# Performance work log

Hardware: AMD Instinct MI355X
Metric: run time of the kernel (lower is better)

## Reference

```python
import jax, jax.numpy as jnp
import numpy as np

D = 256          # embedding_dim
P = 16           # padding_size (patch size, divides D)
CE = 32          # cnn_embedding_dim
HP = 4           # patch_attention_heads
HS = 4           # spatial_temporal_heads
NP = D // P      # patches per token = 16
CC = CE * HP     # conv out channels = 128


def _ln(x):
    # torch module uses mean/std (unbiased, ddof=1), no eps, no affine
    m = jnp.mean(x, axis=-1, keepdims=True)
    s = jnp.std(x, axis=-1, keepdims=True, ddof=1)
    return (x - m) / s


def setup_inputs() -> dict:
    key = jax.random.key(0)
    ks = jax.random.split(key, 20)
    def lin(k, fan_out, fan_in):
        b = 1.0 / np.sqrt(fan_in)
        kw, kb = jax.random.split(k)
        return (jax.random.uniform(kw, (fan_out, fan_in), jnp.float32, -b, b),
                jax.random.uniform(kb, (fan_out,), jnp.float32, -b, b))
    x = jax.random.normal(ks[0], (32, 512, D), jnp.float32)
    Wq, bq = lin(ks[1], D * HS, D)
    Wk, bk = lin(ks[2], D * HS, D)
    Wv, bv = lin(ks[3], D * HS, D)
    Wlin1, blin1 = lin(ks[4], D, D * HS)
    # Conv1d(1, CC, kernel=P, stride=P) weights flattened to (CC, P)
    Wqc, bqc = lin(ks[5], CC, P)
    Wkc, bkc = lin(ks[6], CC, P)
    Wvl, bvl = lin(ks[7], CC, P)
    Wlo, blo = lin(ks[8], P, CC)
    Wlout, blout = lin(ks[9], D, NP * P)
    return dict(x=x, Wq=Wq, bq=bq, Wk=Wk, bk=bk, Wv=Wv, bv=bv,
                Wlin1=Wlin1, blin1=blin1, Wqc=Wqc, bqc=bqc, Wkc=Wkc, bkc=bkc,
                Wvl=Wvl, bvl=bvl, Wlo=Wlo, blo=blo, Wlout=Wlout, blout=blout)


def reference(x, Wq, bq, Wk, bk, Wv, bv, Wlin1, blin1,
              Wqc, bqc, Wkc, bkc, Wvl, bvl, Wlo, blo, Wlout, blout):
    bs, S, _ = x.shape
    orig_x = x
    # ----- spatial-temporal multi-head attention -----
    def heads(W, b):
        y = x @ W.T + b                      # [bs,S,HS*D]
        return y.reshape(bs, S, HS, D).transpose(0, 2, 1, 3)  # [bs,HS,S,D]
    Q, K, V = heads(Wq, bq), heads(Wk, bk), heads(Wv, bv)
    att = jax.nn.softmax(jnp.einsum('bhsd,bhtd->bhst', Q, K) / D, axis=-1)
    o = jnp.einsum('bhst,bhtd->bhsd', att, V)
    o = o.transpose(0, 2, 1, 3).reshape(bs, S, HS * D)
    x1 = _ln(o @ Wlin1.T + blin1 + orig_x)
    # ----- CNN patch attention (D % P == 0, no pad branch) -----
    orig2 = x1
    xp = x1.reshape(bs * S, NP, P)           # patches per token
    # Conv1d with kernel=stride=P == per-patch linear
    Qc = (xp @ Wqc.T + bqc).reshape(-1, NP, HP, CE).transpose(0, 2, 1, 3)
    Kc = (xp @ Wkc.T + bkc).reshape(-1, NP, HP, CE).transpose(0, 2, 1, 3)
    Vc = (xp @ Wvl.T + bvl).reshape(-1, NP, HP, CE).transpose(0, 2, 1, 3)
    scale = jnp.sqrt(jnp.float32(D))
    am = jax.nn.softmax(jnp.einsum('nhpc,nhqc->nhpq', Qc, Kc) / scale, axis=-1)
    oc = jnp.einsum('nhpq,nhqc->nhpc', am, Vc)
    oc = oc.transpose(0, 2, 1, 3).reshape(-1, NP, HP * CE)
    oc = (oc @ Wlo.T + blo).reshape(-1, NP * P)
    oc = (oc @ Wlout.T + blout).reshape(bs, S, D)
    return _ln(oc + orig2)
```

## Files before the change

kernel.cpp:

```cpp
#include <hip/hip_runtime.h>
#include <hip/hip_bf16.h>
#include <math.h>


typedef __attribute__((ext_vector_type(8))) short bf16x8;
typedef __attribute__((ext_vector_type(4))) float f32x4;

__device__ __forceinline__ float bf_lo(unsigned u){ return __uint_as_float(u << 16); }
__device__ __forceinline__ float bf_hi(unsigned u){ return __uint_as_float(u & 0xFFFF0000u); }
__device__ __forceinline__ unsigned short f2bf(float f){
  unsigned u = __float_as_uint(f);
  return (unsigned short)((u + 0x7FFFu + ((u >> 16) & 1u)) >> 16);
}
__device__ __forceinline__ unsigned pack2bf(float a, float b){
  return (unsigned)f2bf(a) | ((unsigned)f2bf(b) << 16);
}
__device__ __forceinline__ bf16x8 pack8(float a0,float a1,float a2,float a3,
                                        float a4,float a5,float a6,float a7){
  union { bf16x8 v; unsigned u[4]; } t;
  t.u[0]=pack2bf(a0,a1); t.u[1]=pack2bf(a2,a3);
  t.u[2]=pack2bf(a4,a5); t.u[3]=pack2bf(a6,a7);
  return t.v;
}
__device__ __forceinline__ void gld16(const void* g, void* l){
  __builtin_amdgcn_global_load_lds((const __attribute__((address_space(1))) void*)g,
                                   (__attribute__((address_space(3))) void*)l, 16, 0, 0);
}

__global__ __launch_bounds__(256) void k_cvt(const float* __restrict__ src,
                                             unsigned short* __restrict__ dst, int n4)
{
  int i = blockIdx.x * 256 + threadIdx.x;
  if (i < n4){
    float4 v = ((const float4*)src)[i];
    ushort4 o;
    o.x = f2bf(v.x); o.y = f2bf(v.y); o.z = f2bf(v.z); o.w = f2bf(v.w);
    ((ushort4*)dst)[i] = o;
  }
}

__global__ __launch_bounds__(256) void k_packw(
    const float* __restrict__ Wqc, const float* __restrict__ Wkc,
    const float* __restrict__ Wvl, const float* __restrict__ Wlo,
    unsigned short* __restrict__ Wp)
{
  int it = blockIdx.x * 256 + threadIdx.x;
  if (it >= 1792) return;
  int ch = it >> 6, lane = it & 63;
  int g = lane >> 4, li = lane & 15;
  unsigned short o[8];
  if (ch < 24){
    int m = ch >> 3, nc = ch & 7;
    const float* W = (m == 0) ? Wqc : (m == 1 ? Wkc : Wvl);
    int c = nc * 16 + li;
    #pragma unroll
    for (int j = 0; j < 8; ++j){
      int k = g * 8 + j;
      o[j] = (k < 16) ? f2bf(W[c * 16 + k]) : (unsigned short)0;
    }
  } else {
    int kc = ch - 24;
    #pragma unroll
    for (int j = 0; j < 8; ++j){
      int k = kc * 32 + g * 8 + j;
      o[j] = f2bf(Wlo[li * 128 + k]);
    }
  }
  #pragma unroll
  for (int j = 0; j < 8; ++j) Wp[it * 8 + j] = o[j];
}

template<int EPI>
__global__ __launch_bounds__(256) void k_gemm(
    const unsigned short* __restrict__ A,
    const unsigned short* __restrict__ W,
    const float* __restrict__ b0,
    const float* __restrict__ b1,
    const float* __restrict__ b2,
    const float* __restrict__ resid,
    void* __restrict__ outp,
    unsigned short* __restrict__ Kw_,
    unsigned short* __restrict__ Vt_,
    int K)
{
  extern __shared__ char sm[];
  const int tid = threadIdx.x;
  const int wid = tid >> 6, lane = tid & 63;
  const int g = lane >> 4, li = lane & 15;
  const int wm = wid >> 1, wn = wid & 1;
  const int m0 = blockIdx.x << 7, n0 = blockIdx.y << 7;

  const unsigned short* Ab = A + (size_t)m0 * K;
  const unsigned short* Wb = W + (size_t)n0 * K;

  auto stage = [&](char* dst, const unsigned short* src, int k0){
    #pragma unroll
    for (int r = 0; r < 4; ++r){
      int row = (r << 5) + (tid >> 3);
      int cb  = (tid & 7) << 4;
      int cbs = cb ^ ((row & 7) << 4);
      gld16(src + row * K + k0 + (cbs >> 1), dst + (r << 12) + (wid << 10));
    }
  };

  f32x4 acc[4][4];
  #pragma unroll
  for (int mf = 0; mf < 4; ++mf)
    #pragma unroll
    for (int nf = 0; nf < 4; ++nf) acc[mf][nf] = (f32x4){0.f,0.f,0.f,0.f};

  const int nk = K >> 6;
  stage(sm, Ab, 0); stage(sm + 32768, Wb, 0);
  for (int kt = 0; kt < nk; ++kt){
    char* Acur = (kt & 1) ? (sm + 16384) : sm;
    char* Wcur = (kt & 1) ? (sm + 49152) : (sm + 32768);
    if (kt + 1 < nk){
      char* Anxt = (kt & 1) ? sm : (sm + 16384);
      char* Wnxt = (kt & 1) ? (sm + 32768) : (sm + 49152);
      stage(Anxt, Ab, (kt + 1) << 6);
      stage(Wnxt, Wb, (kt + 1) << 6);
    }
    __syncthreads();
    bf16x8 af[2][4], wf[2][4];
    #pragma unroll
    for (int kk = 0; kk < 2; ++kk){
      #pragma unroll
      for (int mf = 0; mf < 4; ++mf){
        int row  = (wm << 6) + (mf << 4) + li;
        int colb = ((kk << 6) + (g << 4)) ^ ((row & 7) << 4);
        af[kk][mf] = *(const bf16x8*)(Acur + (row << 7) + colb);
      }
      #pragma unroll
      for (int nf = 0; nf < 4; ++nf){
        int row  = (wn << 6) + (nf << 4) + li;
        int colb = ((kk << 6) + (g << 4)) ^ ((row & 7) << 4);
        wf[kk][nf] = *(const bf16x8*)(Wcur + (row << 7) + colb);
      }
    }
    #pragma unroll
    for (int kk = 0; kk < 2; ++kk)
      #pragma unroll
      for (int mf = 0; mf < 4; ++mf)
        #pragma unroll
        for (int nf = 0; nf < 4; ++nf)
          acc[mf][nf] = __builtin_amdgcn_mfma_f32_16x16x32_bf16(af[kk][mf], wf[kk][nf], acc[mf][nf], 0, 0, 0);
    __syncthreads();
  }

  if (EPI == 0){
    const int chunk = n0 >> 10;
    const float* bias = (chunk == 0) ? b0 : (chunk == 1 ? b1 : b2);
    const int nq0 = n0 & 1023;
    const int h = nq0 >> 8;
    if (chunk == 2){
      const int b  = m0 >> 9;
      const int bh = (b << 2) + h;
      const int d0g = (nq0 & 255) + (wn << 6);
      const int s0g = (m0 & 511) + (wm << 6);
      char* const TB = sm + (wid << 13);
      #pragma unroll
      for (int nf = 0; nf < 4; ++nf){
        const int dloc = (nf << 4) + li;
        const float bv = bias[nq0 + (wn << 6) + (nf << 4) + li];
        #pragma unroll
        for (int mf = 0; mf < 4; ++mf){
          ushort4 pk;
          pk.x = f2bf(acc[mf][nf][0] + bv); pk.y = f2bf(acc[mf][nf][1] + bv);
          pk.z = f2bf(acc[mf][nf][2] + bv); pk.w = f2bf(acc[mf][nf][3] + bv);
          const int unit = ((mf << 2) + g) ^ (dloc & 7);
          *(ushort4*)(TB + (dloc << 7) + (unit << 3)) = pk;
        }
      }
      __asm__ volatile("s_waitcnt lgkmcnt(0)" ::: "memory");
      __builtin_amdgcn_sched_barrier(0);
      #pragma unroll
      for (int p = 0; p < 8; ++p){
        const int dl = (p << 3) + (lane >> 3);
        const int u0 = (lane & 7) << 1;
        uint2 ua = *(const uint2*)(TB + (dl << 7) + (((u0)     ^ (dl & 7)) << 3));
        uint2 ub = *(const uint2*)(TB + (dl << 7) + (((u0 + 1) ^ (dl & 7)) << 3));
        uint4 vv; vv.x = ua.x; vv.y = ua.y; vv.z = ub.x; vv.w = ub.y;
        *(uint4*)(Vt_ + ((size_t)(bh << 8) + d0g + dl) * 512 + s0g + ((lane & 7) << 3)) = vv;
      }
    } else {
      unsigned short* dst = (chunk == 0) ? (unsigned short*)outp : Kw_;
      #pragma unroll
      for (int nf = 0; nf < 4; ++nf){
        const int nq = nq0 + (wn << 6) + (nf << 4) + li;
        const int d = nq & 255;
        const float bv = bias[nq];
        #pragma unroll
        for (int mf = 0; mf < 4; ++mf){
          const int mbase = m0 + (wm << 6) + (mf << 4) + (g << 2);
          #pragma unroll
          for (int r = 0; r < 4; ++r){
            const int m = mbase + r;
            const int b = m >> 9, s = m & 511;
            dst[(size_t)((((b << 2) + h) << 9) + s) * 256 + d] = f2bf(acc[mf][nf][r] + bv);
          }
        }
      }
    }
  } else {
    float* op = (float*)outp;
    #pragma unroll
    for (int nf = 0; nf < 4; ++nf){
      const int n = n0 + (wn << 6) + (nf << 4) + li;
      const float bv = b0[n];
      #pragma unroll
      for (int mf = 0; mf < 4; ++mf){
        const int mbase = m0 + (wm << 6) + (mf << 4) + (g << 2);
        #pragma unroll
        for (int r = 0; r < 4; ++r){
          const int m = mbase + r;
          op[(size_t)m * 256 + n] = acc[mf][nf][r] + bv + resid[(size_t)m * 256 + n];
        }
      }
    }
  }
}

__global__ __launch_bounds__(512) void k_ln(const float* __restrict__ src,
                                            float* __restrict__ dst)
{
  const int lane = threadIdx.x & 63;
  const int n    = blockIdx.x * 8 + (threadIdx.x >> 6);
  float4 v = *(const float4*)(src + (size_t)n * 256 + lane * 4);
  float sum = v.x + v.y + v.z + v.w;
  #pragma unroll
  for (int mk = 32; mk >= 1; mk >>= 1) sum += __shfl_xor(sum, mk);
  float mean = sum * (1.0f / 256.0f);
  float4 e; e.x = v.x - mean; e.y = v.y - mean; e.z = v.z - mean; e.w = v.w - mean;
  float sq = e.x*e.x + e.y*e.y + e.z*e.z + e.w*e.w;
  #pragma unroll
  for (int mk = 32; mk >= 1; mk >>= 1) sq += __shfl_xor(sq, mk);
  float inv = rsqrtf(sq * (1.0f / 255.0f));
  e.x *= inv; e.y *= inv; e.z *= inv; e.w *= inv;
  *(float4*)(dst + (size_t)n * 256 + lane * 4) = e;
}

__global__ __launch_bounds__(256, 2) void k_attn(const unsigned short* __restrict__ Qw,
                                                 const unsigned short* __restrict__ Kw,
                                                 const unsigned short* __restrict__ Vt,
                                                 unsigned short* __restrict__ Ow)
{
  extern __shared__ char smem[];
  const int tid  = threadIdx.x;
  const int wid  = tid >> 6, lane = tid & 63;
  const int g    = lane >> 4, li = lane & 15;
  const int dd   = blockIdx.x + (blockIdx.y << 2);
  const int nl   = ((dd & 7) << 6) + (dd >> 3);
  const int bh   = nl >> 2;
  const int sblk = (nl & 3) << 7;
  const int q0   = sblk + (wid << 5);

  char* const KB0 = smem;
  char* const VB0 = smem + 32768;

  auto stageK = [&](char* kbuf, int t0){
    const unsigned short* base = Kw + ((size_t)(bh << 9) + t0 + (wid << 3)) * 256;
    char* dst = kbuf + (wid << 12);
    #pragma unroll
    for (int c = 0; c < 4; ++c){
      int r  = (c << 1) + (lane >> 5);
      int cs = ((((lane & 31) << 4) ^ (r << 4)) >> 1);
      gld16(base + (r << 8) + cs, dst + (c << 10));
    }
  };
  auto stageV = [&](char* vbuf, int t0){
    char* dst = vbuf + (wid << 12);
    #pragma unroll
    for (int c = 0; c < 4; ++c){
      int gb   = (wid << 12) + (c << 10) + (lane << 4);
      int row  = gb >> 7;
      int d    = (row << 1) + ((gb >> 6) & 1);
      int slot = ((gb >> 4) & 3) ^ (row & 3);
      gld16(Vt + ((size_t)(bh << 8) + d) * 512 + t0 + (slot << 3), dst + (c << 10));
    }
  };

  bf16x8 qf[2][8];
  #pragma unroll
  for (int q2 = 0; q2 < 2; ++q2){
    const unsigned short* qp = Qw + ((size_t)(bh << 9) + q0 + (q2 << 4) + li) * 256 + (g << 3);
    #pragma unroll
    for (int kk = 0; kk < 8; ++kk)
      qf[q2][kk] = *(const bf16x8*)(qp + (kk << 5));
  }
  stageK(KB0, 0);
  stageV(VB0, 0);

  f32x4 o[16][2];
  #pragma unroll
  for (int df = 0; df < 16; ++df){
    o[df][0] = (f32x4){0.f,0.f,0.f,0.f};
    o[df][1] = (f32x4){0.f,0.f,0.f,0.f};
  }
  float m0 = -3.0e38f, m1 = -3.0e38f, l0 = 0.f, l1 = 0.f;

  const float inv256 = 1.0f / 256.0f;
  const int key   = (li & 7) << 4;
  const int laneA = ((g & 1) << 5) + li;
  const bool tf1  = (g >> 1);

  #pragma unroll 1
  for (int t = 0; t < 16; ++t){
    __syncthreads();
    char* kb = KB0 + ((t & 1) << 14);
    char* vb = VB0 + ((t & 1) << 14);
    if (t < 15){
      stageK(KB0 + (((t + 1) & 1) << 14), (t + 1) << 5);
      stageV(VB0 + (((t + 1) & 1) << 14), (t + 1) << 5);
    }

    f32x4 st[2][2];
    st[0][0] = (f32x4){0,0,0,0}; st[0][1] = (f32x4){0,0,0,0};
    st[1][0] = (f32x4){0,0,0,0}; st[1][1] = (f32x4){0,0,0,0};
    #pragma unroll
    for (int kk = 0; kk < 8; ++kk){
      const int colb = ((kk << 6) + (g << 4)) ^ key;
      bf16x8 kf0 = *(const bf16x8*)(kb + (li << 9) + colb);
      bf16x8 kf1 = *(const bf16x8*)(kb + ((16 + li) << 9) + colb);
      st[0][0] = __builtin_amdgcn_mfma_f32_16x16x32_bf16(kf0, qf[0][kk], st[0][0], 0, 0, 0);
      st[0][1] = __builtin_amdgcn_mfma_f32_16x16x32_bf16(kf0, qf[1][kk], st[0][1], 0, 0, 0);
      st[1][0] = __builtin_amdgcn_mfma_f32_16x16x32_bf16(kf1, qf[0][kk], st[1][0], 0, 0, 0);
      st[1][1] = __builtin_amdgcn_mfma_f32_16x16x32_bf16(kf1, qf[1][kk], st[1][1], 0, 0, 0);
    }

    float e0[8], e1[8];
    #pragma unroll
    for (int tf = 0; tf < 2; ++tf)
      #pragma unroll
      for (int r = 0; r < 4; ++r){
        e0[tf*4+r] = st[tf][0][r] * inv256;
        e1[tf*4+r] = st[tf][1][r] * inv256;
      }
    float p0 = e0[0], p1 = e1[0];
    #pragma unroll
    for (int i = 1; i < 8; ++i){ p0 = fmaxf(p0, e0[i]); p1 = fmaxf(p1, e1[i]); }
    p0 = fmaxf(p0, __shfl_xor(p0, 16)); p0 = fmaxf(p0, __shfl_xor(p0, 32));
    p1 = fmaxf(p1, __shfl_xor(p1, 16)); p1 = fmaxf(p1, __shfl_xor(p1, 32));
    if (!__all((p0 - m0 <= 8.0f) && (p1 - m1 <= 8.0f))){
      float mn0 = fmaxf(m0, p0), mn1 = fmaxf(m1, p1);
      float c0 = __expf(m0 - mn0), c1 = __expf(m1 - mn1);
      l0 *= c0; l1 *= c1;
      #pragma unroll
      for (int df = 0; df < 16; ++df){ o[df][0] *= c0; o[df][1] *= c1; }
      m0 = mn0; m1 = mn1;
    }
    float ps0 = 0.f, ps1 = 0.f;
    #pragma unroll
    for (int i = 0; i < 8; ++i){
      e0[i] = __expf(e0[i] - m0); ps0 += e0[i];
      e1[i] = __expf(e1[i] - m1); ps1 += e1[i];
    }
    ps0 += __shfl_xor(ps0, 16); ps0 += __shfl_xor(ps0, 32);
    ps1 += __shfl_xor(ps1, 16); ps1 += __shfl_xor(ps1, 32);
    l0 += ps0; l1 += ps1;

    bf16x8 pf[2];
    #pragma unroll
    for (int q2 = 0; q2 < 2; ++q2){
      const float* e = (q2 == 0) ? e0 : e1;
      unsigned A0 = pack2bf(e[0], e[1]), B0 = pack2bf(e[2], e[3]);
      unsigned A1 = pack2bf(e[4], e[5]), B1 = pack2bf(e[6], e[7]);
      unsigned x0 = __shfl(A0, laneA), x1 = __shfl(B0, laneA);
      unsigned x2 = __shfl(A1, laneA), x3 = __shfl(B1, laneA);
      unsigned y0 = __shfl(A0, laneA + 16), y1 = __shfl(B0, laneA + 16);
      unsigned y2 = __shfl(A1, laneA + 16), y3 = __shfl(B1, laneA + 16);
      union { unsigned u[4]; bf16x8 v; } r;
      r.u[0] = tf1 ? x2 : x0; r.u[1] = tf1 ? x3 : x1;
      r.u[2] = tf1 ? y2 : y0; r.u[3] = tf1 ? y3 : y1;
      pf[q2] = r.v;
    }

    #pragma unroll
    for (int df = 0; df < 16; ++df){
      const int d   = (df << 4) + li;
      const int row = d >> 1;
      bf16x8 va = *(const bf16x8*)(vb + (row << 7) + ((d & 1) << 6) + (((g ^ row) & 3) << 4));
      o[df][0] = __builtin_amdgcn_mfma_f32_16x16x32_bf16(va, pf[0], o[df][0], 0, 0, 0);
      o[df][1] = __builtin_amdgcn_mfma_f32_16x16x32_bf16(va, pf[1], o[df][1], 0, 0, 0);
    }
  }
  __syncthreads();

  float iv0 = 1.0f / l0, iv1 = 1.0f / l1;
  #pragma unroll
  for (int df = 0; df < 16; ++df){ o[df][0] *= iv0; o[df][1] *= iv1; }

  char* const OT = smem + (wid << 13);
  const int b = bh >> 2, h = bh & 3;
  #pragma unroll
  for (int q2 = 0; q2 < 2; ++q2){
    #pragma unroll
    for (int df = 0; df < 16; ++df){
      f32x4 c = o[df][q2];
      uint2 pk; pk.x = pack2bf(c[0], c[1]); pk.y = pack2bf(c[2], c[3]);
      const int addr = (li << 9) + (((df << 5) + (g << 3)) ^ ((li & 7) << 4));
      *(uint2*)(OT + addr) = pk;
    }
    __asm__ volatile("s_waitcnt lgkmcnt(0)" ::: "memory");
    __builtin_amdgcn_sched_barrier(0);
    #pragma unroll
    for (int p = 0; p < 8; ++p){
      const int idx = (p << 6) + lane;
      const int row = idx >> 5, c16 = idx & 31;
      uint4 vv = *(const uint4*)(OT + (row << 9) + (((c16 << 4)) ^ ((row & 7) << 4)));
      const int q = q0 + (q2 << 4) + row;
      *(uint4*)(Ow + ((size_t)((b << 9) + q)) * 1024 + (h << 8) + (c16 << 3)) = vv;
    }
    __asm__ volatile("s_waitcnt lgkmcnt(0)" ::: "memory");
    __builtin_amdgcn_sched_barrier(0);
  }
}

__global__ __launch_bounds__(256) void k_patch2(
    const float* __restrict__ x1,
    const unsigned short* __restrict__ Wp,
    const float* __restrict__ bqc, const float* __restrict__ bkc,
    const float* __restrict__ bvl, const float* __restrict__ blo,
    unsigned short* __restrict__ yb)
{
  extern __shared__ char lds[];
  const int tid = threadIdx.x;
  const int wid = tid >> 6, lane = tid & 63;
  const int g = lane >> 4, li = lane & 15;
  const int n = (blockIdx.x << 2) + wid;

  char* const QB = lds + (wid << 14);
  char* const KB = QB + 4096;
  char* const VB = QB + 8192;
  char* const PB = QB + 14336;
  const int swz = (li & 7) << 4;
  const bf16x8 zf = (bf16x8){0,0,0,0,0,0,0,0};

  bf16x8 xf = zf;
  if (g < 2){
    const float* xr = x1 + (size_t)n * 256 + li * 16 + g * 8;
    float4 a = *(const float4*)xr;
    float4 b = *(const float4*)(xr + 4);
    xf = pack8(a.x,a.y,a.z,a.w, b.x,b.y,b.z,b.w);
  }

  #pragma unroll
  for (int m = 0; m < 3; ++m){
    const float* bias = (m == 0) ? bqc : ((m == 1) ? bkc : bvl);
    #pragma unroll
    for (int nc = 0; nc < 8; ++nc){
      bf16x8 wf = *(const bf16x8*)(Wp + ((((m << 3) + nc) << 6) + lane) * 8);
      f32x4 c = __builtin_amdgcn_mfma_f32_16x16x32_bf16(xf, wf, (f32x4){0,0,0,0}, 0, 0, 0);
      float bv = bias[(nc << 4) + li];
      if (m < 2){
        char* B = (m == 0) ? QB : KB;
        #pragma unroll
        for (int r = 0; r < 4; ++r){
          int p = (g << 2) + r;
          *(unsigned short*)(B + (p << 8) + (((((nc << 4) + li) << 1)) ^ ((p & 7) << 4))) = f2bf(c[r] + bv);
        }
      } else {
        int cc = (nc << 4) + li;
        *(unsigned*)(VB + cc * 48 + (g << 3))     = pack2bf(c[0] + bv, c[1] + bv);
        *(unsigned*)(VB + cc * 48 + (g << 3) + 4) = pack2bf(c[2] + bv, c[3] + bv);
      }
    }
  }
  __asm__ volatile("s_waitcnt lgkmcnt(0)" ::: "memory");
  __builtin_amdgcn_sched_barrier(0);

  f32x4 of[8];
  #pragma unroll
  for (int i = 0; i < 8; ++i) of[i] = (f32x4){0,0,0,0};

  #pragma unroll
  for (int h = 0; h < 4; ++h){
    const int cb = (h << 6) + (g << 4);
    bf16x8 kf = *(const bf16x8*)(KB + (li << 8) + (cb ^ swz));
    bf16x8 qf = *(const bf16x8*)(QB + (li << 8) + (cb ^ swz));
    f32x4 st = __builtin_amdgcn_mfma_f32_16x16x32_bf16(kf, qf, (f32x4){0,0,0,0}, 0, 0, 0);
    float s0 = st[0]*0.0625f, s1 = st[1]*0.0625f, s2 = st[2]*0.0625f, s3 = st[3]*0.0625f;
    float mx = fmaxf(fmaxf(s0, s1), fmaxf(s2, s3));
    mx = fmaxf(mx, __shfl_xor(mx, 16));
    mx = fmaxf(mx, __shfl_xor(mx, 32));
    float e0 = __expf(s0-mx), e1 = __expf(s1-mx), e2 = __expf(s2-mx), e3 = __expf(s3-mx);
    float ss = e0 + e1 + e2 + e3;
    ss += __shfl_xor(ss, 16);
    ss += __shfl_xor(ss, 32);
    float inv = 1.0f / ss;
    e0 *= inv; e1 *= inv; e2 *= inv; e3 *= inv;
    *(unsigned*)(PB + li * 80 + (g << 3))     = pack2bf(e0, e1);
    *(unsigned*)(PB + li * 80 + (g << 3) + 4) = pack2bf(e2, e3);
    __asm__ volatile("s_waitcnt lgkmcnt(0)" ::: "memory");
    __builtin_amdgcn_sched_barrier(0);
    bf16x8 pf = zf;
    if (g < 2) pf = *(const bf16x8*)(PB + li * 80 + (g << 4));
    #pragma unroll
    for (int t = 0; t < 2; ++t){
      bf16x8 vf = zf;
      if (g < 2) vf = *(const bf16x8*)(VB + ((h << 5) + (t << 4) + li) * 48 + (g << 4));
      of[(h << 1) + t] = __builtin_amdgcn_mfma_f32_16x16x32_bf16(pf, vf, of[(h << 1) + t], 0, 0, 0);
    }
  }

  #pragma unroll
  for (int h = 0; h < 4; ++h)
    #pragma unroll
    for (int t = 0; t < 2; ++t){
      f32x4 c = of[(h << 1) + t];
      int cc = (h << 5) + (t << 4) + li;
      #pragma unroll
      for (int r = 0; r < 4; ++r){
        int p = (g << 2) + r;
        *(unsigned short*)(QB + (p << 8) + ((cc << 1) ^ ((p & 7) << 4))) = f2bf(c[r]);
      }
    }
  __asm__ volatile("s_waitcnt lgkmcnt(0)" ::: "memory");
  __builtin_amdgcn_sched_barrier(0);

  f32x4 y = (f32x4){0,0,0,0};
  #pragma unroll
  for (int kc = 0; kc < 4; ++kc){
    bf16x8 af = *(const bf16x8*)(QB + (li << 8) + ((((kc << 6) + (g << 4))) ^ swz));
    bf16x8 wf = *(const bf16x8*)(Wp + (((24 + kc) << 6) + lane) * 8);
    y = __builtin_amdgcn_mfma_f32_16x16x32_bf16(af, wf, y, 0, 0, 0);
  }
  float bv = blo[li];
  unsigned short* yr = yb + (size_t)n * 256 + li;
  #pragma unroll
  for (int r = 0; r < 4; ++r)
    yr[((g << 2) + r) << 4] = f2bf(y[r] + bv);
}

extern "C" void kernel_launch(void* const* d_in, const int* in_sizes, int n_in,
                              void* d_out, int out_size, void* d_ws, size_t ws_size,
                              hipStream_t stream)
{
  const float* x     = (const float*)d_in[0];
  const float* Wq    = (const float*)d_in[1];
  const float* bq    = (const float*)d_in[2];
  const float* Wk    = (const float*)d_in[3];
  const float* bk    = (const float*)d_in[4];
  const float* Wv    = (const float*)d_in[5];
  const float* bv    = (const float*)d_in[6];
  const float* Wlin1 = (const float*)d_in[7];
  const float* blin1 = (const float*)d_in[8];
  const float* Wqc   = (const float*)d_in[9];
  const float* bqc   = (const float*)d_in[10];
  const float* Wkc   = (const float*)d_in[11];
  const float* bkc   = (const float*)d_in[12];
  const float* Wvl   = (const float*)d_in[13];
  const float* bvl   = (const float*)d_in[14];
  const float* Wlo   = (const float*)d_in[15];
  const float* blo   = (const float*)d_in[16];
  const float* Wlout = (const float*)d_in[17];
  const float* blout = (const float*)d_in[18];
  float* out = (float*)d_out;

  char* w = (char*)d_ws;
  unsigned short* Qw  = (unsigned short*)w;
  unsigned short* yb  = (unsigned short*)w;
  unsigned short* Kw  = (unsigned short*)(w + 33554432);
  unsigned short* xb  = (unsigned short*)(w + 100663296);
  unsigned short* Ow  = (unsigned short*)(w + 100663296);
  unsigned short* Vtw = (unsigned short*)(w + 134217728);
  float* x1raw  = (float*)(w + 134217728);
  float* outraw = (float*)(w + 134217728);
  float* x1     = (float*)(w + 150994944);
  unsigned short* Wqkvb  = (unsigned short*)(w + 167772160);
  unsigned short* Wlin1b = (unsigned short*)(w + 169345024);
  unsigned short* Wloutb = (unsigned short*)(w + 169869312);
  unsigned short* Wp     = (unsigned short*)(w + 170000384);

  hipFuncSetAttribute((const void*)k_attn, hipFuncAttributeMaxDynamicSharedMemorySize, 65536);
  hipFuncSetAttribute((const void*)k_gemm<0>, hipFuncAttributeMaxDynamicSharedMemorySize, 65536);
  hipFuncSetAttribute((const void*)k_gemm<1>, hipFuncAttributeMaxDynamicSharedMemorySize, 65536);
  hipFuncSetAttribute((const void*)k_patch2, hipFuncAttributeMaxDynamicSharedMemorySize, 65536);

  k_cvt<<<4096, 256, 0, stream>>>(x, xb, 1048576);
  k_cvt<<<256, 256, 0, stream>>>(Wq, Wqkvb, 65536);
  k_cvt<<<256, 256, 0, stream>>>(Wk, Wqkvb + 262144, 65536);
  k_cvt<<<256, 256, 0, stream>>>(Wv, Wqkvb + 524288, 65536);
  k_cvt<<<256, 256, 0, stream>>>(Wlin1, Wlin1b, 65536);
  k_cvt<<<64, 256, 0, stream>>>(Wlout, Wloutb, 16384);
  k_packw<<<7, 256, 0, stream>>>(Wqc, Wkc, Wvl, Wlo, Wp);

  k_gemm<0><<<dim3(128, 24), 256, 65536, stream>>>(xb, Wqkvb, bq, bk, bv,
                                                   nullptr, Qw, Kw, Vtw, 256);
  k_attn<<<dim3(4, 128), 256, 65536, stream>>>(Qw, Kw, Vtw, Ow);

  k_gemm<1><<<dim3(128, 2), 256, 65536, stream>>>(Ow, Wlin1b, blin1, nullptr, nullptr,
                                                  x, x1raw, nullptr, nullptr, 1024);
  k_ln<<<2048, 512, 0, stream>>>(x1raw, x1);

  k_patch2<<<4096, 256, 65536, stream>>>(x1, Wp, bqc, bkc, bvl, blo, yb);

  k_gemm<1><<<dim3(128, 2), 256, 65536, stream>>>(yb, Wloutb, blout, nullptr, nullptr,
                                                  x1, outraw, nullptr, nullptr, 256);
  k_ln<<<2048, 512, 0, stream>>>(outraw, out);
}
```

Measured before the change: 221.6 us.

## Fuse output GEMMs with residual-add LayerNorm and trim patch-attention LDS traffic

Adds a k_gemm_ln kernel whose 64-row tile spans the full 256-wide output. It adds bias and residual, then computes the row LayerNorm in the epilogue using cross-lane shuffles and a small LDS table. This removes the fp32 round-trip and the two separate LN launches. Separately, the patch kernel now passes softmax probabilities between lanes with shuffles instead of an LDS scratch buffer, and the attention MFMA loops are wrapped in s_setprio. Risks: the fused GEMM launches only 256 blocks, which may underfill the GPU, and variance is computed as E[x²]−mean², which is less numerically stable.

```diff
diff --git a/kernel.cpp b/kernel.cpp
--- a/kernel.cpp
+++ b/kernel.cpp
@@ -6,8 +6,6 @@
 typedef __attribute__((ext_vector_type(8))) short bf16x8;
 typedef __attribute__((ext_vector_type(4))) float f32x4;
 
-__device__ __forceinline__ float bf_lo(unsigned u){ return __uint_as_float(u << 16); }
-__device__ __forceinline__ float bf_hi(unsigned u){ return __uint_as_float(u & 0xFFFF0000u); }
 __device__ __forceinline__ unsigned short f2bf(float f){
   unsigned u = __float_as_uint(f);
   return (unsigned short)((u + 0x7FFFu + ((u >> 16) & 1u)) >> 16);
@@ -77,7 +75,6 @@
     const float* __restrict__ b0,
     const float* __restrict__ b1,
     const float* __restrict__ b2,
-    const float* __restrict__ resid,
     void* __restrict__ outp,
     unsigned short* __restrict__ Kw_,
     unsigned short* __restrict__ Vt_,
@@ -147,96 +144,180 @@
     __syncthreads();
   }
 
-  if (EPI == 0){
-    const int chunk = n0 >> 10;
-    const float* bias = (chunk == 0) ? b0 : (chunk == 1 ? b1 : b2);
-    const int nq0 = n0 & 1023;
-    const int h = nq0 >> 8;
-    if (chunk == 2){
-      const int b  = m0 >> 9;
-      const int bh = (b << 2) + h;
-      const int d0g = (nq0 & 255) + (wn << 6);
-      const int s0g = (m0 & 511) + (wm << 6);
-      char* const TB = sm + (wid << 13);
-      #pragma unroll
-      for (int nf = 0; nf < 4; ++nf){
-        const int dloc = (nf << 4) + li;
-        const float bv = bias[nq0 + (wn << 6) + (nf << 4) + li];
-        #pragma unroll
-        for (int mf = 0; mf < 4; ++mf){
-          ushort4 pk;
-          pk.x = f2bf(acc[mf][nf][0] + bv); pk.y = f2bf(acc[mf][nf][1] + bv);
-          pk.z = f2bf(acc[mf][nf][2] + bv); pk.w = f2bf(acc[mf][nf][3] + bv);
-          const int unit = ((mf << 2) + g) ^ (dloc & 7);
-          *(ushort4*)(TB + (dloc << 7) + (unit << 3)) = pk;
-        }
-      }
-      __asm__ volatile("s_waitcnt lgkmcnt(0)" ::: "memory");
-      __builtin_amdgcn_sched_barrier(0);
-      #pragma unroll
-      for (int p = 0; p < 8; ++p){
-        const int dl = (p << 3) + (lane >> 3);
-        const int u0 = (lane & 7) << 1;
-        uint2 ua = *(const uint2*)(TB + (dl << 7) + (((u0)     ^ (dl & 7)) << 3));
-        uint2 ub = *(const uint2*)(TB + (dl << 7) + (((u0 + 1) ^ (dl & 7)) << 3));
-        uint4 vv; vv.x = ua.x; vv.y = ua.y; vv.z = ub.x; vv.w = ub.y;
-        *(uint4*)(Vt_ + ((size_t)(bh << 8) + d0g + dl) * 512 + s0g + ((lane & 7) << 3)) = vv;
-      }
-    } else {
-      unsigned short* dst = (chunk == 0) ? (unsigned short*)outp : Kw_;
-      #pragma unroll
-      for (int nf = 0; nf < 4; ++nf){
-        const int nq = nq0 + (wn << 6) + (nf << 4) + li;
-        const int d = nq & 255;
-        const float bv = bias[nq];
-        #pragma unroll
-        for (int mf = 0; mf < 4; ++mf){
-          const int mbase = m0 + (wm << 6) + (mf << 4) + (g << 2);
-          #pragma unroll
-          for (int r = 0; r < 4; ++r){
-            const int m = mbase + r;
-            const int b = m >> 9, s = m & 511;
-            dst[(size_t)((((b << 2) + h) << 9) + s) * 256 + d] = f2bf(acc[mf][nf][r] + bv);
-          }
-        }
-      }
+  const int chunk = n0 >> 10;
+  const float* bias = (chunk == 0) ? b0 : (chunk == 1 ? b1 : b2);
+  const int nq0 = n0 & 1023;
+  const int h = nq0 >> 8;
+  if (chunk == 2){
+    const int b  = m0 >> 9;
+    const int bh = (b << 2) + h;
+    const int d0g = (nq0 & 255) + (wn << 6);
+    const int s0g = (m0 & 511) + (wm << 6);
+    char* const TB = sm + (wid << 13);
+    #pragma unroll
+    for (int nf = 0; nf < 4; ++nf){
+      const int dloc = (nf << 4) + li;
+      const float bv = bias[nq0 + (wn << 6) + (nf << 4) + li];
+      #pragma unroll
+      for (int mf = 0; mf < 4; ++mf){
+        ushort4 pk;
+        pk.x = f2bf(acc[mf][nf][0] + bv); pk.y = f2bf(acc[mf][nf][1] + bv);
+        pk.z = f2bf(acc[mf][nf][2] + bv); pk.w = f2bf(acc[mf][nf][3] + bv);
+        const int unit = ((mf << 2) + g) ^ (dloc & 7);
+        *(ushort4*)(TB + (dloc << 7) + (unit << 3)) = pk;
+      }
+    }
+    __asm__ volatile("s_waitcnt lgkmcnt(0)" ::: "memory");
+    __builtin_amdgcn_sched_barrier(0);
+    #pragma unroll
+    for (int p = 0; p < 8; ++p){
+      const int dl = (p << 3) + (lane >> 3);
+      const int u0 = (lane & 7) << 1;
+      uint2 ua = *(const uint2*)(TB + (dl << 7) + (((u0)     ^ (dl & 7)) << 3));
+      uint2 ub = *(const uint2*)(TB + (dl << 7) + (((u0 + 1) ^ (dl & 7)) << 3));
+      uint4 vv; vv.x = ua.x; vv.y = ua.y; vv.z = ub.x; vv.w = ub.y;
+      *(uint4*)(Vt_ + ((size_t)(bh << 8) + d0g + dl) * 512 + s0g + ((lane & 7) << 3)) = vv;
     }
   } else {
-    float* op = (float*)outp;
+    unsigned short* dst = (chunk == 0) ? (unsigned short*)outp : Kw_;
     #pragma unroll
     for (int nf = 0; nf < 4; ++nf){
-      const int n = n0 + (wn << 6) + (nf << 4) + li;
-      const float bv = b0[n];
+      const int nq = nq0 + (wn << 6) + (nf << 4) + li;
+      const int d = nq & 255;
+      const float bv = bias[nq];
       #pragma unroll
       for (int mf = 0; mf < 4; ++mf){
         const int mbase = m0 + (wm << 6) + (mf << 4) + (g << 2);
         #pragma unroll
         for (int r = 0; r < 4; ++r){
           const int m = mbase + r;
-          op[(size_t)m * 256 + n] = acc[mf][nf][r] + bv + resid[(size_t)m * 256 + n];
+          const int b = m >> 9, s = m & 511;
+          dst[(size_t)((((b << 2) + h) << 9) + s) * 256 + d] = f2bf(acc[mf][nf][r] + bv);
         }
       }
     }
   }
 }
 
-__global__ __launch_bounds__(512) void k_ln(const float* __restrict__ src,
-                                            float* __restrict__ dst)
+__global__ __launch_bounds__(256) void k_gemm_ln(
+    const unsigned short* __restrict__ A,
+    const unsigned short* __restrict__ W,
+    const float* __restrict__ bias,
+    const float* __restrict__ resid,
+    float* __restrict__ outp,
+    int K)
 {
-  const int lane = threadIdx.x & 63;
-  const int n    = blockIdx.x * 8 + (threadIdx.x >> 6);
-  float4 v = *(const float4*)(src + (size_t)n * 256 + lane * 4);
-  float sum = v.x + v.y + v.z + v.w;
-  #pragma unroll
-  for (int mk = 32; mk >= 1; mk >>= 1) sum += __shfl_xor(sum, mk);
-  float mean = sum * (1.0f / 256.0f);
-  float4 e; e.x = v.x - mean; e.y = v.y - mean; e.z = v.z - mean; e.w = v.w - mean;
-  float sq = e.x*e.x + e.y*e.y + e.z*e.z + e.w*e.w;
-  #pragma unroll
-  for (int mk = 32; mk >= 1; mk >>= 1) sq += __shfl_xor(sq, mk);
-  float inv = rsqrtf(sq * (1.0f / 255.0f));
-  e.x *= inv; e.y *= inv; e.z *= inv; e.w *= inv;
-  *(float4*)(dst + (size_t)n * 256 + lane * 4) = e;
+  extern __shared__ char sm[];
+  const int tid = threadIdx.x;
+  const int wid = tid >> 6, lane = tid & 63;
+  const int g = lane >> 4, li = lane & 15;
+  const int m0 = blockIdx.x << 6;
+  const unsigned short* Ab = A + (size_t)m0 * K;
+
+  auto stageA = [&](char* dst, int k0){
+    int row = tid >> 2;
+    int cs  = (tid & 3) ^ (row & 3);
+    gld16(Ab + (size_t)row * K + k0 + (cs << 3), dst + (wid << 10));
+  };
+  auto stageW = [&](char* dst, int k0){
+    #pragma unroll
+    for (int cc = 0; cc < 4; ++cc){
+      int u = (cc << 8) + tid;
+      int row = u >> 2;
+      int cs  = (u & 3) ^ (row & 3);
+      gld16(W + (size_t)row * K + k0 + (cs << 3), dst + (cc << 12) + (wid << 10));
+    }
+  };
+
+  f32x4 acc[4][4];
+  #pragma unroll
+  for (int mf = 0; mf < 4; ++mf)
+    #pragma unroll
+    for (int nf = 0; nf < 4; ++nf) acc[mf][nf] = (f32x4){0.f,0.f,0.f,0.f};
+
+  const int nk = K >> 5;
+  stageA(sm, 0); stageW(sm + 8192, 0);
+  for (int kt = 0; kt < nk; ++kt){
+    char* Acur = (kt & 1) ? (sm + 4096)  : sm;
+    char* Wcur = (kt & 1) ? (sm + 24576) : (sm + 8192);
+    if (kt + 1 < nk){
+      stageA((kt & 1) ? sm : (sm + 4096), (kt + 1) << 5);
+      stageW((kt & 1) ? (sm + 8192) : (sm + 24576), (kt + 1) << 5);
+    }
+    __syncthreads();
+    bf16x8 af[4], wf[4];
+    #pragma unroll
+    for (int mf = 0; mf < 4; ++mf){
+      int row  = (mf << 4) + li;
+      int colb = (g << 4) ^ ((row & 3) << 4);
+      af[mf] = *(const bf16x8*)(Acur + (row << 6) + colb);
+    }
+    #pragma unroll
+    for (int nf = 0; nf < 4; ++nf){
+      int row  = (wid << 6) + (nf << 4) + li;
+      int colb = (g << 4) ^ ((row & 3) << 4);
+      wf[nf] = *(const bf16x8*)(Wcur + (row << 6) + colb);
+    }
+    #pragma unroll
+    for (int mf = 0; mf < 4; ++mf)
+      #pragma unroll
+      for (int nf = 0; nf < 4; ++nf)
+        acc[mf][nf] = __builtin_amdgcn_mfma_f32_16x16x32_bf16(af[mf], wf[nf], acc[mf][nf], 0, 0, 0);
+    __syncthreads();
+  }
+
+  float bv[4];
+  #pragma unroll
+  for (int nf = 0; nf < 4; ++nf) bv[nf] = bias[(wid << 6) + (nf << 4) + li];
+  #pragma unroll
+  for (int mf = 0; mf < 4; ++mf)
+    #pragma unroll
+    for (int r = 0; r < 4; ++r){
+      const int m = (mf << 4) + (g << 2) + r;
+      #pragma unroll
+      for (int nf = 0; nf < 4; ++nf)
+        acc[mf][nf][r] += bv[nf] + resid[(size_t)(m0 + m) * 256 + (wid << 6) + (nf << 4) + li];
+    }
+
+  float2* tbl = (float2*)sm;
+  #pragma unroll
+  for (int mf = 0; mf < 4; ++mf)
+    #pragma unroll
+    for (int r = 0; r < 4; ++r){
+      float ps = 0.f, pq = 0.f;
+      #pragma unroll
+      for (int nf = 0; nf < 4; ++nf){
+        float v = acc[mf][nf][r];
+        ps += v; pq += v * v;
+      }
+      #pragma unroll
+      for (int mk = 1; mk <= 8; mk <<= 1){
+        ps += __shfl_xor(ps, mk); pq += __shfl_xor(pq, mk);
+      }
+      if (li == 0){
+        float2 e; e.x = ps; e.y = pq;
+        tbl[(wid << 6) + (mf << 4) + (g << 2) + r] = e;
+      }
+    }
+  __syncthreads();
+  #pragma unroll
+  for (int mf = 0; mf < 4; ++mf)
+    #pragma unroll
+    for (int r = 0; r < 4; ++r){
+      const int m = (mf << 4) + (g << 2) + r;
+      float s = 0.f, q = 0.f;
+      #pragma unroll
+      for (int w = 0; w < 4; ++w){
+        float2 e = tbl[(w << 6) + m];
+        s += e.x; q += e.y;
+      }
+      float mean = s * (1.0f / 256.0f);
+      float inv  = rsqrtf((q - 256.0f * mean * mean) * (1.0f / 255.0f));
+      #pragma unroll
+      for (int nf = 0; nf < 4; ++nf)
+        outp[(size_t)(m0 + m) * 256 + (wid << 6) + (nf << 4) + li] =
+            (acc[mf][nf][r] - mean) * inv;
+    }
 }
 
 __global__ __launch_bounds__(256, 2) void k_attn(const unsigned short* __restrict__ Qw,
@@ -316,6 +397,7 @@
     f32x4 st[2][2];
     st[0][0] = (f32x4){0,0,0,0}; st[0][1] = (f32x4){0,0,0,0};
     st[1][0] = (f32x4){0,0,0,0}; st[1][1] = (f32x4){0,0,0,0};
+    __builtin_amdgcn_s_setprio(1);
     #pragma unroll
     for (int kk = 0; kk < 8; ++kk){
       const int colb = ((kk << 6) + (g << 4)) ^ key;
@@ -326,6 +408,7 @@
       st[1][0] = __builtin_amdgcn_mfma_f32_16x16x32_bf16(kf1, qf[0][kk], st[1][0], 0, 0, 0);
       st[1][1] = __builtin_amdgcn_mfma_f32_16x16x32_bf16(kf1, qf[1][kk], st[1][1], 0, 0, 0);
     }
+    __builtin_amdgcn_s_setprio(0);
 
     float e0[8], e1[8];
     #pragma unroll
@@ -374,6 +457,7 @@
       pf[q2] = r.v;
     }
 
+    __builtin_amdgcn_s_setprio(1);
     #pragma unroll
     for (int df = 0; df < 16; ++df){
       const int d   = (df << 4) + li;
@@ -382,6 +466,7 @@
       o[df][0] = __builtin_amdgcn_mfma_f32_16x16x32_bf16(va, pf[0], o[df][0], 0, 0, 0);
       o[df][1] = __builtin_amdgcn_mfma_f32_16x16x32_bf16(va, pf[1], o[df][1], 0, 0, 0);
     }
+    __builtin_amdgcn_s_setprio(0);
   }
   __syncthreads();
 
@@ -431,7 +516,6 @@
   char* const QB = lds + (wid << 14);
   char* const KB = QB + 4096;
   char* const VB = QB + 8192;
-  char* const PB = QB + 14336;
   const int swz = (li & 7) << 4;
   const bf16x8 zf = (bf16x8){0,0,0,0,0,0,0,0};
 
@@ -468,32 +552,44 @@
   __asm__ volatile("s_waitcnt lgkmcnt(0)" ::: "memory");
   __builtin_amdgcn_sched_barrier(0);
 
-  f32x4 of[8];
-  #pragma unroll
-  for (int i = 0; i < 8; ++i) of[i] = (f32x4){0,0,0,0};
-
+  f32x4 st[4];
   #pragma unroll
   for (int h = 0; h < 4; ++h){
     const int cb = (h << 6) + (g << 4);
     bf16x8 kf = *(const bf16x8*)(KB + (li << 8) + (cb ^ swz));
     bf16x8 qf = *(const bf16x8*)(QB + (li << 8) + (cb ^ swz));
-    f32x4 st = __builtin_amdgcn_mfma_f32_16x16x32_bf16(kf, qf, (f32x4){0,0,0,0}, 0, 0, 0);
-    float s0 = st[0]*0.0625f, s1 = st[1]*0.0625f, s2 = st[2]*0.0625f, s3 = st[3]*0.0625f;
+    st[h] = __builtin_amdgcn_mfma_f32_16x16x32_bf16(kf, qf, (f32x4){0,0,0,0}, 0, 0, 0);
+  }
+
+  float e[4][4];
+  #pragma unroll
+  for (int h = 0; h < 4; ++h){
+    float s0 = st[h][0]*0.0625f, s1 = st[h][1]*0.0625f,
+          s2 = st[h][2]*0.0625f, s3 = st[h][3]*0.0625f;
     float mx = fmaxf(fmaxf(s0, s1), fmaxf(s2, s3));
     mx = fmaxf(mx, __shfl_xor(mx, 16));
     mx = fmaxf(mx, __shfl_xor(mx, 32));
-    float e0 = __expf(s0-mx), e1 = __expf(s1-mx), e2 = __expf(s2-mx), e3 = __expf(s3-mx);
-    float ss = e0 + e1 + e2 + e3;
+    float v0 = __expf(s0-mx), v1 = __expf(s1-mx), v2 = __expf(s2-mx), v3 = __expf(s3-mx);
+    float ss = v0 + v1 + v2 + v3;
     ss += __shfl_xor(ss, 16);
     ss += __shfl_xor(ss, 32);
     float inv = 1.0f / ss;
-    e0 *= inv; e1 *= inv; e2 *= inv; e3 *= inv;
-    *(unsigned*)(PB + li * 80 + (g << 3))     = pack2bf(e0, e1);
-    *(unsigned*)(PB + li * 80 + (g << 3) + 4) = pack2bf(e2, e3);
-    __asm__ volatile("s_waitcnt lgkmcnt(0)" ::: "memory");
-    __builtin_amdgcn_sched_barrier(0);
-    bf16x8 pf = zf;
-    if (g < 2) pf = *(const bf16x8*)(PB + li * 80 + (g << 4));
+    e[h][0] = v0*inv; e[h][1] = v1*inv; e[h][2] = v2*inv; e[h][3] = v3*inv;
+  }
+
+  const int laneA = ((g & 1) << 5) + li;
+  f32x4 of[8];
+  #pragma unroll
+  for (int i = 0; i < 8; ++i) of[i] = (f32x4){0,0,0,0};
+  #pragma unroll
+  for (int h = 0; h < 4; ++h){
+    unsigned pk0 = pack2bf(e[h][0], e[h][1]);
+    unsigned pk1 = pack2bf(e[h][2], e[h][3]);
+    unsigned u0 = __shfl(pk0, laneA),      u1 = __shfl(pk1, laneA);
+    unsigned u2 = __shfl(pk0, laneA + 16), u3 = __shfl(pk1, laneA + 16);
+    union { unsigned u[4]; bf16x8 v; } pr;
+    pr.u[0] = u0; pr.u[1] = u1; pr.u[2] = u2; pr.u[3] = u3;
+    bf16x8 pf = (g < 2) ? pr.v : zf;
     #pragma unroll
     for (int t = 0; t < 2; ++t){
       bf16x8 vf = zf;
@@ -502,6 +598,8 @@
     }
   }
 
+  __asm__ volatile("s_waitcnt lgkmcnt(0)" ::: "memory");
+  __builtin_amdgcn_sched_barrier(0);
   #pragma unroll
   for (int h = 0; h < 4; ++h)
     #pragma unroll
@@ -511,7 +609,7 @@
       #pragma unroll
       for (int r = 0; r < 4; ++r){
         int p = (g << 2) + r;
-        *(unsigned short*)(QB + (p << 8) + ((cc << 1) ^ ((p & 7) << 4))) = f2bf(c[r]);
+        *(unsigned short*)(KB + (p << 8) + ((cc << 1) ^ ((p & 7) << 4))) = f2bf(c[r]);
       }
     }
   __asm__ volatile("s_waitcnt lgkmcnt(0)" ::: "memory");
@@ -520,7 +618,7 @@
   f32x4 y = (f32x4){0,0,0,0};
   #pragma unroll
   for (int kc = 0; kc < 4; ++kc){
-    bf16x8 af = *(const bf16x8*)(QB + (li << 8) + ((((kc << 6) + (g << 4))) ^ swz));
+    bf16x8 af = *(const bf16x8*)(KB + (li << 8) + ((((kc << 6) + (g << 4))) ^ swz));
     bf16x8 wf = *(const bf16x8*)(Wp + (((24 + kc) << 6) + lane) * 8);
     y = __builtin_amdgcn_mfma_f32_16x16x32_bf16(af, wf, y, 0, 0, 0);
   }
@@ -563,8 +661,6 @@
   unsigned short* xb  = (unsigned short*)(w + 100663296);
   unsigned short* Ow  = (unsigned short*)(w + 100663296);
   unsigned short* Vtw = (unsigned short*)(w + 134217728);
-  float* x1raw  = (float*)(w + 134217728);
-  float* outraw = (float*)(w + 134217728);
   float* x1     = (float*)(w + 150994944);
   unsigned short* Wqkvb  = (unsigned short*)(w + 167772160);
   unsigned short* Wlin1b = (unsigned short*)(w + 169345024);
@@ -573,7 +669,7 @@
 
   hipFuncSetAttribute((const void*)k_attn, hipFuncAttributeMaxDynamicSharedMemorySize, 65536);
   hipFuncSetAttribute((const void*)k_gemm<0>, hipFuncAttributeMaxDynamicSharedMemorySize, 65536);
-  hipFuncSetAttribute((const void*)k_gemm<1>, hipFuncAttributeMaxDynamicSharedMemorySize, 65536);
+  hipFuncSetAttribute((const void*)k_gemm_ln, hipFuncAttributeMaxDynamicSharedMemorySize, 40960);
   hipFuncSetAttribute((const void*)k_patch2, hipFuncAttributeMaxDynamicSharedMemorySize, 65536);
 
   k_cvt<<<4096, 256, 0, stream>>>(x, xb, 1048576);
@@ -585,16 +681,12 @@
   k_packw<<<7, 256, 0, stream>>>(Wqc, Wkc, Wvl, Wlo, Wp);
 
   k_gemm<0><<<dim3(128, 24), 256, 65536, stream>>>(xb, Wqkvb, bq, bk, bv,
-                                                   nullptr, Qw, Kw, Vtw, 256);
+                                                   Qw, Kw, Vtw, 256);
   k_attn<<<dim3(4, 128), 256, 65536, stream>>>(Qw, Kw, Vtw, Ow);
 
-  k_gemm<1><<<dim3(128, 2), 256, 65536, stream>>>(Ow, Wlin1b, blin1, nullptr, nullptr,
-                                                  x, x1raw, nullptr, nullptr, 1024);
-  k_ln<<<2048, 512, 0, stream>>>(x1raw, x1);
+  k_gemm_ln<<<256, 256, 40960, stream>>>(Ow, Wlin1b, blin1, x, x1, 1024);
 
   k_patch2<<<4096, 256, 65536, stream>>>(x1, Wp, bqc, bkc, bvl, blo, yb);
 
-  k_gemm<1><<<dim3(128, 2), 256, 65536, stream>>>(yb, Wloutb, blout, nullptr, nullptr,
-                                                  x1, outraw, nullptr, nullptr, 256);
-  k_ln<<<2048, 512, 0, stream>>>(outraw, out);
-}
+  k_gemm_ln<<<256, 256, 40960, stream>>>(yb, Wloutb, blout, x1, out, 256);
+}
```

New measurement: 220.7 us. No clear change (-0.4%).
